# Kernel optimization log

Hardware: AMD Instinct MI355X
Metric: run time of the kernel (lower is better)

The kernel has to match this reference:

```python
import jax, jax.numpy as jnp
import numpy as np

DIM = 1024
N_EXPERTS = 8
TOPK = 2
INTER = 1408
SHARED_INTER = 2 * INTER  # n_shared_experts * moe_inter_dim
BATCH, SEQ = 2, 1024


def setup_inputs() -> dict:
    key = jax.random.key(0)
    ks = jax.random.split(key, 16)
    s = 0.02
    f32 = jnp.float32
    return {
        "x": jax.random.normal(ks[0], (BATCH, SEQ, DIM), f32),
        # gate
        "gate_w": jax.random.normal(ks[1], (N_EXPERTS, DIM), f32) * s,
        "gate_b": jnp.zeros((N_EXPERTS,), f32),
        # stacked routed-expert weights (nn.Linear layout: [out, in])
        "w1": jax.random.normal(ks[2], (N_EXPERTS, INTER, DIM), f32) * s,
        "b1": jnp.zeros((N_EXPERTS, INTER), f32),
        "w2": jax.random.normal(ks[3], (N_EXPERTS, DIM, INTER), f32) * s,
        "b2": jnp.zeros((N_EXPERTS, DIM), f32),
        "w3": jax.random.normal(ks[4], (N_EXPERTS, INTER, DIM), f32) * s,
        "b3": jnp.zeros((N_EXPERTS, INTER), f32),
        # shared-expert MLP
        "sw1": jax.random.normal(ks[5], (SHARED_INTER, DIM), f32) * s,
        "sb1": jnp.zeros((SHARED_INTER,), f32),
        "sw2": jax.random.normal(ks[6], (DIM, SHARED_INTER), f32) * s,
        "sb2": jnp.zeros((DIM,), f32),
        "sw3": jax.random.normal(ks[7], (SHARED_INTER, DIM), f32) * s,
        "sb3": jnp.zeros((SHARED_INTER,), f32),
    }


def reference(x, gate_w, gate_b, w1, b1, w2, b2, w3, b3,
              sw1, sb1, sw2, sb2, sw3, sb3):
    shape = x.shape
    xf = x.reshape(-1, shape[-1])  # [T, D]

    # Gate (returns full probs + top-k indices, matching source)
    scores = xf @ gate_w.T + gate_b                      # [T, E]
    probs = jax.nn.softmax(scores, axis=-1)              # [T, E]
    _, idx = jax.lax.top_k(probs, TOPK)                  # [T, K] int32

    # Faithful to `weights[mask].sum(dim=1)` where weights == full probs
    scale = probs.sum(axis=-1, keepdims=True)            # [T, 1] (== 1 for softmax)

    # dispatch[t, e] = token t routed to expert e
    dispatch = (idx[:, :, None] == jnp.arange(N_EXPERTS)[None, None, :]).any(axis=1)  # [T, E]

    # Dense per-expert SwiGLU (mask-combine mirrors the source's masked loop)
    h1 = jnp.einsum('td,eid->tei', xf, w1) + b1          # [T, E, I]
    h3 = jnp.einsum('td,eid->tei', xf, w3) + b3          # [T, E, I]
    out = jnp.einsum('tei,edi->ted', jax.nn.silu(h1) * h3, w2) + b2  # [T, E, D]
    y = jnp.where(dispatch[:, :, None], out, 0.0).sum(axis=1) * scale  # [T, D]

    # Shared-expert MLP
    z = (jax.nn.silu(xf @ sw1.T + sb1) * (xf @ sw3.T + sb3)) @ sw2.T + sb2  # [T, D]

    return probs, idx, (y + z).reshape(shape)
```

## Files before the change

### kernel.cpp

```cpp
#include <hip/hip_runtime.h>
#include <math.h>

static constexpr int TOK    = 2048;
static constexpr int DIM_   = 1024;
static constexpr int NE     = 8;
static constexpr int INTER_ = 1408;
static constexpr int SINT   = 2816;
static constexpr int NSLOT  = TOK * 2;

static constexpr size_t XB_OFF   = 0;
static constexpr size_t HR_OFF   = XB_OFF   + (size_t)TOK * DIM_ * 2;
static constexpr size_t HS_OFF   = HR_OFF   + (size_t)NSLOT * INTER_ * 2;
static constexpr size_t YS_OFF   = HS_OFF   + (size_t)TOK * SINT * 2;
static constexpr size_t ZP_OFF   = YS_OFF   + (size_t)NSLOT * DIM_ * 2;
static constexpr size_t W1B_OFF  = ZP_OFF   + (size_t)2 * TOK * DIM_ * 4;
static constexpr size_t W3B_OFF  = W1B_OFF  + (size_t)NE * INTER_ * DIM_ * 2;
static constexpr size_t W2B_OFF  = W3B_OFF  + (size_t)NE * INTER_ * DIM_ * 2;
static constexpr size_t SW1B_OFF = W2B_OFF  + (size_t)NE * DIM_ * INTER_ * 2;
static constexpr size_t SW3B_OFF = SW1B_OFF + (size_t)SINT * DIM_ * 2;
static constexpr size_t SW2B_OFF = SW3B_OFF + (size_t)SINT * DIM_ * 2;
static constexpr size_t TOPK_OFF = SW2B_OFF + (size_t)DIM_ * SINT * 2;
static constexpr size_t SCALE_OFF= TOPK_OFF + (size_t)TOK * 2 * 4;
static constexpr size_t SLOT_OFF = SCALE_OFF+ (size_t)TOK * 4;
static constexpr size_t ROWT_OFF = SLOT_OFF + (size_t)TOK * 2 * 4;
static constexpr size_t WL_OFF   = ROWT_OFF + (size_t)NSLOT * 4 + 1024;

typedef unsigned short u16;
typedef u16   u16x4  __attribute__((ext_vector_type(4)));
typedef u16   u16x8  __attribute__((ext_vector_type(8)));
typedef __bf16 bf16x8 __attribute__((ext_vector_type(8)));
typedef float f32x4  __attribute__((ext_vector_type(4)));

static __device__ __forceinline__ u16 f2bf(float f) {
  unsigned int u = __builtin_bit_cast(unsigned int, f);
  return (u16)((u + 0x7fffu + ((u >> 16) & 1u)) >> 16);
}
static __device__ __forceinline__ float bf2f(u16 h) {
  unsigned int u = ((unsigned int)h) << 16;
  return __builtin_bit_cast(float, u);
}
static __device__ __forceinline__ f32x4 mfma16(u16x8 a, u16x8 b, f32x4 c) {
  return __builtin_amdgcn_mfma_f32_16x16x32_bf16(
      __builtin_bit_cast(bf16x8, a), __builtin_bit_cast(bf16x8, b), c, 0, 0, 0);
}
static __device__ __forceinline__ void gload16(const void* g, void* l) {
  __builtin_amdgcn_global_load_lds(
      (const __attribute__((address_space(1))) unsigned int*)g,
      (__attribute__((address_space(3))) unsigned int*)l, 16, 0, 0);
}
#define WAITV(N) asm volatile("s_waitcnt vmcnt(" #N ")" ::: "memory")

__global__ __launch_bounds__(256) void gate_conv_kernel(
    const float* __restrict__ x, const float* __restrict__ gw,
    const float* __restrict__ gb,
    const float* __restrict__ w1, const float* __restrict__ w3,
    const float* __restrict__ sw1, const float* __restrict__ sw3,
    u16* __restrict__ xb, u16* __restrict__ w1b, u16* __restrict__ w3b,
    u16* __restrict__ sw1b, u16* __restrict__ sw3b,
    float* __restrict__ probs_out, float* __restrict__ idx_out,
    int* __restrict__ topk, float* __restrict__ scalep)
{
  const int tid = threadIdx.x;
  if (blockIdx.x >= 512) {
    int g = blockIdx.x - 512;
    const float* src; u16* dst;
    if      (g < 2816) {            src = w1;  dst = w1b;  }
    else if (g < 5632) { g -= 2816; src = w3;  dst = w3b;  }
    else if (g < 6336) { g -= 5632; src = sw1; dst = sw1b; }
    else               { g -= 6336; src = sw3; dst = sw3b; }
    const size_t base = (size_t)g * 4096 + (size_t)tid * 16;
    #pragma unroll
    for (int j = 0; j < 4; ++j) {
      float4 v = *(const float4*)(src + base + j * 4);
      *(u16x4*)(dst + base + j * 4) =
          (u16x4){ f2bf(v.x), f2bf(v.y), f2bf(v.z), f2bf(v.w) };
    }
    return;
  }
  {
    const size_t base = (size_t)blockIdx.x * 4096 + (size_t)tid * 16;
    const float4* src = (const float4*)(x + base);
    u16* dst = xb + base;
    #pragma unroll
    for (int j = 0; j < 4; ++j) {
      float4 v = src[j];
      *(u16x4*)(dst + j * 4) = (u16x4){ f2bf(v.x), f2bf(v.y), f2bf(v.z), f2bf(v.w) };
    }
  }
  const int wid = tid >> 6, lane = tid & 63;
  const int t = blockIdx.x * 4 + wid;
  const float* xr = x + (size_t)t * DIM_;
  double part[NE] = {0,0,0,0,0,0,0,0};
  for (int it = 0; it < DIM_ / 64; ++it) {
    const int d = lane + it * 64;
    const double xv = (double)xr[d];
    #pragma unroll
    for (int e = 0; e < NE; ++e) part[e] += xv * (double)gw[e * DIM_ + d];
  }
  #pragma unroll
  for (int e = 0; e < NE; ++e) {
    #pragma unroll
    for (int off = 32; off; off >>= 1) part[e] += __shfl_xor(part[e], off);
    part[e] += (double)gb[e];
  }
  if (lane == 0) {
    double m = part[0];
    #pragma unroll
    for (int e = 1; e < NE; ++e) m = fmax(m, part[e]);
    double p[NE], sd = 0.0;
    #pragma unroll
    for (int e = 0; e < NE; ++e) { p[e] = exp(part[e] - m); sd += p[e]; }
    float pf[NE]; float sumf = 0.0f;
    #pragma unroll
    for (int e = 0; e < NE; ++e) { pf[e] = (float)(p[e] / sd); sumf += pf[e]; }
    int a0 = 0;
    #pragma unroll
    for (int e = 1; e < NE; ++e) if (part[e] > part[a0]) a0 = e;
    int a1 = (a0 == 0) ? 1 : 0;
    #pragma unroll
    for (int e = 0; e < NE; ++e) if (e != a0 && part[e] > part[a1]) a1 = e;
    #pragma unroll
    for (int e = 0; e < NE; ++e) probs_out[t * NE + e] = pf[e];
    idx_out[t * 2 + 0] = (float)a0;
    idx_out[t * 2 + 1] = (float)a1;
    topk[t * 2 + 0] = a0; topk[t * 2 + 1] = a1;
    scalep[t] = sumf;
  }
}

__global__ __launch_bounds__(256) void plan_kernel(
    const int* __restrict__ topk, int4* __restrict__ wl,
    int* __restrict__ row_token, int* __restrict__ slot_of)
{
  __shared__ int pc[256][NE];
  __shared__ int base[NE], tot[NE];
  const int tid = threadIdx.x;
  int loc[NE] = {0,0,0,0,0,0,0,0};
  #pragma unroll 1
  for (int i = 0; i < 16; ++i) ++loc[topk[tid * 16 + i]];
  #pragma unroll
  for (int e = 0; e < NE; ++e) pc[tid][e] = loc[e];
  __syncthreads();
  if (tid < NE) {
    int acc = 0;
    for (int th = 0; th < 256; ++th) { int v = pc[th][tid]; pc[th][tid] = acc; acc += v; }
    tot[tid] = acc;
  }
  __syncthreads();
  if (tid == 0) {
    int acc = 0;
    for (int e = 0; e < NE; ++e) { base[e] = acc; acc += tot[e]; }
    int n = 0;
    for (int e = 0; e < NE; ++e)
      for (int r = 0; r < tot[e]; r += 256)
        wl[n++] = make_int4(e, base[e] + r, min(256, tot[e] - r), 0);
    for (int h = 0; h < 2; ++h)
      for (int mt = 0; mt < 8; ++mt)
        wl[n++] = make_int4(NE + h, mt * 256, 256, 0);
    for (int i = n; i < 64; ++i) wl[i] = make_int4(-1, 0, 0, 0);
  }
  __syncthreads();
  int pos[NE];
  #pragma unroll
  for (int e = 0; e < NE; ++e) pos[e] = base[e] + pc[tid][e];
  #pragma unroll 1
  for (int i = 0; i < 16; ++i) {
    const int gi = tid * 16 + i;
    const int e = topk[gi];
    const int s = pos[e]++;
    row_token[s] = gi >> 1;
    slot_of[gi] = s;
  }
}

__global__ __launch_bounds__(512) void g13_kernel(
    const u16* __restrict__ xb, const int* __restrict__ row_token,
    const int4* __restrict__ wl,
    const u16* __restrict__ w1b, const float* __restrict__ b1,
    const u16* __restrict__ w3b, const float* __restrict__ b3,
    const u16* __restrict__ sw1b, const float* __restrict__ sb1,
    const u16* __restrict__ sw3b, const float* __restrict__ sb3,
    u16* __restrict__ Hr, u16* __restrict__ Hs,
    const float* __restrict__ w2f, const float* __restrict__ sw2f,
    u16* __restrict__ w2b, u16* __restrict__ sw2b)
{
  constexpr int K = DIM_;
  constexpr int NT = K / 32;
  const int tid = threadIdx.x, wid = tid >> 6, lane = tid & 63;

  if (blockIdx.y >= 40) {
    const int cid = (blockIdx.y - 40) * 22 + blockIdx.x;
    for (int chunk = cid; chunk < 1760; chunk += 176) {
      int g = chunk; const float* src; u16* dst;
      if (g < 1408) { src = w2f;  dst = w2b;  }
      else { g -= 1408; src = sw2f; dst = sw2b; }
      const size_t base = (size_t)g * 8192 + (size_t)tid * 16;
      #pragma unroll
      for (int j = 0; j < 4; ++j) {
        float4 v = *(const float4*)(src + base + j * 4);
        *(u16x4*)(dst + base + j * 4) =
            (u16x4){ f2bf(v.x), f2bf(v.y), f2bf(v.z), f2bf(v.w) };
      }
    }
    return;
  }

  const int4 it = wl[blockIdx.y];
  const int z = it.x;
  if (z < 0) return;
  const int rowbase = it.y, rows_lim = it.z;
  const int col0 = blockIdx.x * 64;

  const int lrow = lane >> 2;
  const int sce = ((lane & 3) ^ ((lane >> 3) & 3)) * 8;

  const u16 *W1, *W3; const float *B1p, *B3p;
  u16* Hbase; int ldh;
  const u16* aptr[2];

  if (z < NE) {
    #pragma unroll
    for (int q = 0; q < 2; ++q) {
      const int rq = wid * 32 + q * 16 + lrow;
      const int t = (rq < rows_lim) ? row_token[rowbase + rq] : 0;
      aptr[q] = xb + (size_t)t * K + sce;
    }
    W1 = w1b + (size_t)z * INTER_ * K;  W3 = w3b + (size_t)z * INTER_ * K;
    B1p = b1 + z * INTER_;              B3p = b3 + z * INTER_;
    Hbase = Hr + (size_t)rowbase * INTER_;  ldh = INTER_;
  } else {
    const int h = z - NE;
    #pragma unroll
    for (int q = 0; q < 2; ++q) {
      const int rq = wid * 32 + q * 16 + lrow;
      aptr[q] = xb + (size_t)(rowbase + min(rq, rows_lim - 1)) * K + sce;
    }
    W1 = sw1b + (size_t)h * INTER_ * K;  W3 = sw3b + (size_t)h * INTER_ * K;
    B1p = sb1 + h * INTER_;              B3p = sb3 + h * INTER_;
    Hbase = Hs + (size_t)rowbase * SINT + h * INTER_;  ldh = SINT;
  }

  __shared__ alignas(16) u16 Al [2][256 * 32];
  __shared__ alignas(16) u16 B1l[2][64 * 32];
  __shared__ alignas(16) u16 B3l[2][64 * 32];

  const int brole = wid >> 2, bw = wid & 3;
  const u16* bsrc = (brole ? W3 : W1) + (size_t)(col0 + bw * 16 + lrow) * K + sce;
  u16* bdst0 = brole ? &B3l[0][bw * 512] : &B1l[0][bw * 512];
  u16* bdst1 = brole ? &B3l[1][bw * 512] : &B1l[1][bw * 512];

  #define G13_STAGE(p, kt) {                                          \
    const int k0_ = (kt) * 32;                                        \
    gload16(aptr[0] + k0_, &Al[p][(wid * 2 + 0) * 512]);              \
    gload16(aptr[1] + k0_, &Al[p][(wid * 2 + 1) * 512]);              \
    gload16(bsrc + k0_, (p) ? bdst1 : bdst0);                         \
  }

  G13_STAGE(0, 0);

  const int wr = wid >> 1, wc = wid & 1, fr = lane & 15, gr = lane >> 4;
  const int key = (fr >> 1) & 3;
  f32x4 acc1[4][2] = {}, acc3[4][2] = {};
  int p = 0;

  #pragma unroll 1
  for (int kt = 0; kt < NT; ++kt) {
    if (kt + 1 < NT) { G13_STAGE(p ^ 1, kt + 1); WAITV(3); }
    else             { WAITV(0); }
    __builtin_amdgcn_s_barrier();
    u16x8 af[4], b1f[2], b3f[2];
    #pragma unroll
    for (int mi = 0; mi < 4; ++mi)
      af[mi] = *(const u16x8*)&Al[p][(wr * 64 + mi * 16 + fr) * 32 + ((gr ^ key) * 8)];
    #pragma unroll
    for (int ni = 0; ni < 2; ++ni) {
      const int off = (wc * 32 + ni * 16 + fr) * 32 + ((gr ^ key) * 8);
      b1f[ni] = *(const u16x8*)&B1l[p][off];
      b3f[ni] = *(const u16x8*)&B3l[p][off];
    }
    __builtin_amdgcn_s_setprio(1);
    #pragma unroll
    for (int mi = 0; mi < 4; ++mi)
      #pragma unroll
      for (int ni = 0; ni < 2; ++ni) {
        acc1[mi][ni] = mfma16(af[mi], b1f[ni], acc1[mi][ni]);
        acc3[mi][ni] = mfma16(af[mi], b3f[ni], acc3[mi][ni]);
      }
    __builtin_amdgcn_s_setprio(0);
    __builtin_amdgcn_s_barrier();
    p ^= 1;
  }
  #undef G13_STAGE

  #pragma unroll
  for (int ni = 0; ni < 2; ++ni) {
    const int gcol = col0 + wc * 32 + ni * 16 + fr;
    const float bb1 = B1p[gcol], bb3 = B3p[gcol];
    #pragma unroll
    for (int mi = 0; mi < 4; ++mi) {
      const int rb = wr * 64 + mi * 16 + gr * 4;
      #pragma unroll
      for (int j = 0; j < 4; ++j) {
        const int r = rb + j;
        if (r < rows_lim) {
          const float h1 = acc1[mi][ni][j] + bb1;
          const float h3 = acc3[mi][ni][j] + bb3;
          const float hv = (h1 / (1.0f + __expf(-h1))) * h3;
          Hbase[(size_t)r * ldh + gcol] = f2bf(hv);
        }
      }
    }
  }
}

__global__ __launch_bounds__(512) void g2_kernel(
    const u16* __restrict__ Hr, const u16* __restrict__ Hs,
    const int4* __restrict__ wl,
    const u16* __restrict__ w2b, const float* __restrict__ b2,
    const u16* __restrict__ sw2b,
    u16* __restrict__ Ys, float* __restrict__ Zp)
{
  constexpr int NT = INTER_ / 32;
  const int4 it = wl[blockIdx.y];
  const int z = it.x;
  if (z < 0) return;
  const int rowbase = it.y, rows_lim = it.z;
  const int col0 = blockIdx.x * 128;

  const int tid = threadIdx.x, wid = tid >> 6, lane = tid & 63;
  const int lrow = lane >> 2;
  const int sce = ((lane & 3) ^ ((lane >> 3) & 3)) * 8;

  const u16 *Abase, *W; const float* BB;
  int ldA, ldW;
  u16* Yout = nullptr; float* Zout = nullptr;
  if (z < NE) {
    Abase = Hr + (size_t)rowbase * INTER_;  ldA = INTER_;
    W = w2b + (size_t)z * DIM_ * INTER_;    ldW = INTER_;
    BB = b2 + z * DIM_;
    Yout = Ys + (size_t)rowbase * DIM_;
  } else {
    const int h = z - NE;
    Abase = Hs + (size_t)rowbase * SINT + h * INTER_;  ldA = SINT;
    W = sw2b + h * INTER_;                             ldW = SINT;
    BB = nullptr;
    Zout = Zp + (size_t)h * TOK * DIM_ + (size_t)rowbase * DIM_;
  }

  const u16* aptr[2];
  #pragma unroll
  for (int q = 0; q < 2; ++q) {
    const int rq = wid * 32 + q * 16 + lrow;
    aptr[q] = Abase + (size_t)min(rq, rows_lim - 1) * ldA + sce;
  }
  const u16* wsrc = W + (size_t)(col0 + wid * 16 + lrow) * ldW + sce;

  __shared__ alignas(16) u16 Al[3][256 * 32];
  __shared__ alignas(16) u16 Bl[3][128 * 32];

  #define G2_STAGE(p, kt) {                                           \
    const int k0_ = (kt) * 32;                                        \
    gload16(aptr[0] + k0_, &Al[p][(wid * 2 + 0) * 512]);              \
    gload16(aptr[1] + k0_, &Al[p][(wid * 2 + 1) * 512]);              \
    gload16(wsrc + k0_, &Bl[p][wid * 512]);                           \
  }

  G2_STAGE(0, 0);
  G2_STAGE(1, 1);

  const int wr = wid >> 1, wc = wid & 1, fr = lane & 15, gr = lane >> 4;
  const int key = (fr >> 1) & 3;
  f32x4 acc[4][4] = {};
  int cur = 0;

  #pragma unroll 1
  for (int kt = 0; kt < NT; ++kt) {
    if (kt + 1 < NT) { WAITV(3); }
    else             { WAITV(0); }
    __builtin_amdgcn_s_barrier();
    if (kt + 2 < NT) {
      const int nx = (cur + 2 >= 3) ? cur - 1 : cur + 2;
      G2_STAGE(nx, kt + 2);
    }
    u16x8 af[4], bf_[4];
    #pragma unroll
    for (int mi = 0; mi < 4; ++mi)
      af[mi] = *(const u16x8*)&Al[cur][(wr * 64 + mi * 16 + fr) * 32 + ((gr ^ key) * 8)];
    #pragma unroll
    for (int ni = 0; ni < 4; ++ni)
      bf_[ni] = *(const u16x8*)&Bl[cur][(wc * 64 + ni * 16 + fr) * 32 + ((gr ^ key) * 8)];
    __builtin_amdgcn_s_setprio(1);
    #pragma unroll
    for (int mi = 0; mi < 4; ++mi)
      #pragma unroll
      for (int ni = 0; ni < 4; ++ni)
        acc[mi][ni] = mfma16(af[mi], bf_[ni], acc[mi][ni]);
    __builtin_amdgcn_s_setprio(0);
    cur = (cur + 1 == 3) ? 0 : cur + 1;
  }
  #undef G2_STAGE

  #pragma unroll
  for (int ni = 0; ni < 4; ++ni) {
    const int gcol = col0 + wc * 64 + ni * 16 + fr;
    const float bb = BB ? BB[gcol] : 0.0f;
    #pragma unroll
    for (int mi = 0; mi < 4; ++mi) {
      const int rb = wr * 64 + mi * 16 + gr * 4;
      #pragma unroll
      for (int j = 0; j < 4; ++j) {
        const int r = rb + j;
        if (r < rows_lim) {
          const float val = acc[mi][ni][j] + bb;
          if (z < NE) Yout[(size_t)r * DIM_ + gcol] = f2bf(val);
          else        Zout[(size_t)r * DIM_ + gcol] = val;
        }
      }
    }
  }
}

__global__ __launch_bounds__(256) void combine_kernel(
    const u16* __restrict__ Ys, const float* __restrict__ Zp,
    const int* __restrict__ slot_of, const float* __restrict__ scalep,
    const float* __restrict__ sb2, float* __restrict__ y_out)
{
  const int t = blockIdx.x, c = threadIdx.x * 4;
  const int s0 = slot_of[t * 2], s1 = slot_of[t * 2 + 1];
  const float s = scalep[t];
  u16x4 a = *(const u16x4*)(Ys + (size_t)s0 * DIM_ + c);
  u16x4 b = *(const u16x4*)(Ys + (size_t)s1 * DIM_ + c);
  float4 z0 = *(const float4*)(Zp + (size_t)t * DIM_ + c);
  float4 z1 = *(const float4*)(Zp + (size_t)TOK * DIM_ + (size_t)t * DIM_ + c);
  float4 sb = *(const float4*)(sb2 + c);
  float4 o;
  o.x = (bf2f(a[0]) + bf2f(b[0])) * s + z0.x + z1.x + sb.x;
  o.y = (bf2f(a[1]) + bf2f(b[1])) * s + z0.y + z1.y + sb.y;
  o.z = (bf2f(a[2]) + bf2f(b[2])) * s + z0.z + z1.z + sb.z;
  o.w = (bf2f(a[3]) + bf2f(b[3])) * s + z0.w + z1.w + sb.w;
  *(float4*)(y_out + (size_t)t * DIM_ + c) = o;
}

extern "C" void kernel_launch(void* const* d_in, const int* in_sizes, int n_in,
                              void* d_out, int out_size, void* d_ws, size_t ws_size,
                              hipStream_t stream) {
  (void)in_sizes; (void)n_in; (void)out_size; (void)ws_size;
  const float* x   = (const float*)d_in[0];
  const float* gw  = (const float*)d_in[1];
  const float* gb  = (const float*)d_in[2];
  const float* w1  = (const float*)d_in[3];
  const float* b1  = (const float*)d_in[4];
  const float* w2  = (const float*)d_in[5];
  const float* b2  = (const float*)d_in[6];
  const float* w3  = (const float*)d_in[7];
  const float* b3  = (const float*)d_in[8];
  const float* sw1 = (const float*)d_in[9];
  const float* sb1 = (const float*)d_in[10];
  const float* sw2 = (const float*)d_in[11];
  const float* sb2 = (const float*)d_in[12];
  const float* sw3 = (const float*)d_in[13];
  const float* sb3 = (const float*)d_in[14];

  float* out       = (float*)d_out;
  float* probs_out = out;
  float* idx_out   = out + TOK * NE;
  float* y_out     = out + TOK * NE + TOK * 2;

  char* ws = (char*)d_ws;
  u16*   xb        = (u16*)  (ws + XB_OFF);
  u16*   Hr        = (u16*)  (ws + HR_OFF);
  u16*   Hs        = (u16*)  (ws + HS_OFF);
  u16*   Ysl       = (u16*)  (ws + YS_OFF);
  float* Zp        = (float*)(ws + ZP_OFF);
  u16*   w1b       = (u16*)  (ws + W1B_OFF);
  u16*   w3b       = (u16*)  (ws + W3B_OFF);
  u16*   w2b       = (u16*)  (ws + W2B_OFF);
  u16*   sw1b      = (u16*)  (ws + SW1B_OFF);
  u16*   sw3b      = (u16*)  (ws + SW3B_OFF);
  u16*   sw2b      = (u16*)  (ws + SW2B_OFF);
  int*   topk      = (int*)  (ws + TOPK_OFF);
  float* scalep    = (float*)(ws + SCALE_OFF);
  int*   slot_of   = (int*)  (ws + SLOT_OFF);
  int*   row_token = (int*)  (ws + ROWT_OFF);
  int4*  wl        = (int4*) (ws + WL_OFF);

  gate_conv_kernel<<<512 + 7040, 256, 0, stream>>>(
      x, gw, gb, w1, w3, sw1, sw3,
      xb, w1b, w3b, sw1b, sw3b,
      probs_out, idx_out, topk, scalep);
  plan_kernel<<<1, 256, 0, stream>>>(topk, wl, row_token, slot_of);
  g13_kernel<<<dim3(22, 48), 512, 0, stream>>>(
      xb, row_token, wl, w1b, b1, w3b, b3, sw1b, sb1, sw3b, sb3, Hr, Hs,
      w2, sw2, w2b, sw2b);
  g2_kernel<<<dim3(8, 40), 512, 0, stream>>>(
      Hr, Hs, wl, w2b, b2, sw2b, Ysl, Zp);
  combine_kernel<<<TOK, 256, 0, stream>>>(Ysl, Zp, slot_of, scalep, sb2, y_out);
}
```

Before: 196.5 us.

## Fuse combine into down-projection via atomic adds with split-K work list

```diff
diff --git a/kernel.cpp b/kernel.cpp
--- a/kernel.cpp
+++ b/kernel.cpp
@@ -7,13 +7,12 @@
 static constexpr int INTER_ = 1408;
 static constexpr int SINT   = 2816;
 static constexpr int NSLOT  = TOK * 2;
+static constexpr int KC     = 704;
 
 static constexpr size_t XB_OFF   = 0;
 static constexpr size_t HR_OFF   = XB_OFF   + (size_t)TOK * DIM_ * 2;
 static constexpr size_t HS_OFF   = HR_OFF   + (size_t)NSLOT * INTER_ * 2;
-static constexpr size_t YS_OFF   = HS_OFF   + (size_t)TOK * SINT * 2;
-static constexpr size_t ZP_OFF   = YS_OFF   + (size_t)NSLOT * DIM_ * 2;
-static constexpr size_t W1B_OFF  = ZP_OFF   + (size_t)2 * TOK * DIM_ * 4;
+static constexpr size_t W1B_OFF  = HS_OFF   + (size_t)TOK * SINT * 2;
 static constexpr size_t W3B_OFF  = W1B_OFF  + (size_t)NE * INTER_ * DIM_ * 2;
 static constexpr size_t W2B_OFF  = W3B_OFF  + (size_t)NE * INTER_ * DIM_ * 2;
 static constexpr size_t SW1B_OFF = W2B_OFF  + (size_t)NE * DIM_ * INTER_ * 2;
@@ -24,6 +23,7 @@
 static constexpr size_t SLOT_OFF = SCALE_OFF+ (size_t)TOK * 4;
 static constexpr size_t ROWT_OFF = SLOT_OFF + (size_t)TOK * 2 * 4;
 static constexpr size_t WL_OFF   = ROWT_OFF + (size_t)NSLOT * 4 + 1024;
+static constexpr size_t WL2_OFF  = WL_OFF   + 48 * 16;
 
 typedef unsigned short u16;
 typedef u16   u16x4  __attribute__((ext_vector_type(4)));
@@ -58,7 +58,8 @@
     u16* __restrict__ xb, u16* __restrict__ w1b, u16* __restrict__ w3b,
     u16* __restrict__ sw1b, u16* __restrict__ sw3b,
     float* __restrict__ probs_out, float* __restrict__ idx_out,
-    int* __restrict__ topk, float* __restrict__ scalep)
+    int* __restrict__ topk, float* __restrict__ scalep,
+    float* __restrict__ y_out)
 {
   const int tid = threadIdx.x;
   if (blockIdx.x >= 512) {
@@ -78,6 +79,12 @@
     return;
   }
   {
+    float4 z4 = {0.f, 0.f, 0.f, 0.f};
+    float* yz = y_out + (size_t)blockIdx.x * 4096 + (size_t)tid * 16;
+    #pragma unroll
+    for (int j = 0; j < 4; ++j) *(float4*)(yz + j * 4) = z4;
+  }
+  {
     const size_t base = (size_t)blockIdx.x * 4096 + (size_t)tid * 16;
     const float4* src = (const float4*)(x + base);
     u16* dst = xb + base;
@@ -129,7 +136,8 @@
 }
 
 __global__ __launch_bounds__(256) void plan_kernel(
-    const int* __restrict__ topk, int4* __restrict__ wl,
+    const int* __restrict__ topk, int4* __restrict__ wl13,
+    int4* __restrict__ wl2,
     int* __restrict__ row_token, int* __restrict__ slot_of)
 {
   __shared__ int pc[256][NE];
@@ -153,11 +161,20 @@
     int n = 0;
     for (int e = 0; e < NE; ++e)
       for (int r = 0; r < tot[e]; r += 256)
-        wl[n++] = make_int4(e, base[e] + r, min(256, tot[e] - r), 0);
+        wl13[n++] = make_int4(e, base[e] + r, min(256, tot[e] - r), 0);
     for (int h = 0; h < 2; ++h)
       for (int mt = 0; mt < 8; ++mt)
-        wl[n++] = make_int4(NE + h, mt * 256, 256, 0);
-    for (int i = n; i < 64; ++i) wl[i] = make_int4(-1, 0, 0, 0);
+        wl13[n++] = make_int4(NE + h, mt * 256, 256, 0);
+    for (int i = n; i < 48; ++i) wl13[i] = make_int4(-1, 0, 0, 0);
+    int n2 = 0;
+    for (int e = 0; e < NE; ++e)
+      for (int r = 0; r < tot[e]; r += 256)
+        for (int kh = 0; kh < 2; ++kh)
+          wl2[n2++] = make_int4(e, base[e] + r, min(256, tot[e] - r), kh);
+    for (int q = 0; q < 4; ++q)
+      for (int mt = 0; mt < 8; ++mt)
+        wl2[n2++] = make_int4(NE, mt * 256, 256, q);
+    for (int i = n2; i < 80; ++i) wl2[i] = make_int4(-1, 0, 0, 0);
   }
   __syncthreads();
   int pos[NE];
@@ -315,36 +332,32 @@
 
 __global__ __launch_bounds__(512) void g2_kernel(
     const u16* __restrict__ Hr, const u16* __restrict__ Hs,
-    const int4* __restrict__ wl,
+    const int4* __restrict__ wl2, const int* __restrict__ row_token,
+    const float* __restrict__ scalep,
     const u16* __restrict__ w2b, const float* __restrict__ b2,
-    const u16* __restrict__ sw2b,
-    u16* __restrict__ Ys, float* __restrict__ Zp)
+    const u16* __restrict__ sw2b, const float* __restrict__ sb2,
+    float* __restrict__ y_out)
 {
-  constexpr int NT = INTER_ / 32;
-  const int4 it = wl[blockIdx.y];
+  constexpr int NT = KC / 32;
+  const int4 it = wl2[blockIdx.y];
   const int z = it.x;
   if (z < 0) return;
-  const int rowbase = it.y, rows_lim = it.z;
+  const int rowbase = it.y, rows_lim = it.z, kq = it.w;
   const int col0 = blockIdx.x * 128;
 
   const int tid = threadIdx.x, wid = tid >> 6, lane = tid & 63;
   const int lrow = lane >> 2;
   const int sce = ((lane & 3) ^ ((lane >> 3) & 3)) * 8;
 
-  const u16 *Abase, *W; const float* BB;
+  const u16 *Abase, *W;
   int ldA, ldW;
-  u16* Yout = nullptr; float* Zout = nullptr;
-  if (z < NE) {
-    Abase = Hr + (size_t)rowbase * INTER_;  ldA = INTER_;
-    W = w2b + (size_t)z * DIM_ * INTER_;    ldW = INTER_;
-    BB = b2 + z * DIM_;
-    Yout = Ys + (size_t)rowbase * DIM_;
+  const bool routed = (z < NE);
+  if (routed) {
+    Abase = Hr + (size_t)rowbase * INTER_ + kq * KC;          ldA = INTER_;
+    W = w2b + (size_t)z * DIM_ * INTER_ + kq * KC;            ldW = INTER_;
   } else {
-    const int h = z - NE;
-    Abase = Hs + (size_t)rowbase * SINT + h * INTER_;  ldA = SINT;
-    W = sw2b + h * INTER_;                             ldW = SINT;
-    BB = nullptr;
-    Zout = Zp + (size_t)h * TOK * DIM_ + (size_t)rowbase * DIM_;
+    Abase = Hs + (size_t)rowbase * SINT + kq * KC;            ldA = SINT;
+    W = sw2b + kq * KC;                                       ldW = SINT;
   }
 
   const u16* aptr[2];
@@ -403,7 +416,8 @@
   #pragma unroll
   for (int ni = 0; ni < 4; ++ni) {
     const int gcol = col0 + wc * 64 + ni * 16 + fr;
-    const float bb = BB ? BB[gcol] : 0.0f;
+    float bb = 0.0f;
+    if (kq == 0) bb = routed ? b2[z * DIM_ + gcol] : sb2[gcol];
     #pragma unroll
     for (int mi = 0; mi < 4; ++mi) {
       const int rb = wr * 64 + mi * 16 + gr * 4;
@@ -411,34 +425,18 @@
       for (int j = 0; j < 4; ++j) {
         const int r = rb + j;
         if (r < rows_lim) {
-          const float val = acc[mi][ni][j] + bb;
-          if (z < NE) Yout[(size_t)r * DIM_ + gcol] = f2bf(val);
-          else        Zout[(size_t)r * DIM_ + gcol] = val;
+          if (routed) {
+            const int tok = row_token[rowbase + r];
+            atomicAdd(&y_out[(size_t)tok * DIM_ + gcol],
+                      (acc[mi][ni][j] + bb) * scalep[tok]);
+          } else {
+            atomicAdd(&y_out[(size_t)(rowbase + r) * DIM_ + gcol],
+                      acc[mi][ni][j] + bb);
+          }
         }
       }
     }
   }
-}
-
-__global__ __launch_bounds__(256) void combine_kernel(
-    const u16* __restrict__ Ys, const float* __restrict__ Zp,
-    const int* __restrict__ slot_of, const float* __restrict__ scalep,
-    const float* __restrict__ sb2, float* __restrict__ y_out)
-{
-  const int t = blockIdx.x, c = threadIdx.x * 4;
-  const int s0 = slot_of[t * 2], s1 = slot_of[t * 2 + 1];
-  const float s = scalep[t];
-  u16x4 a = *(const u16x4*)(Ys + (size_t)s0 * DIM_ + c);
-  u16x4 b = *(const u16x4*)(Ys + (size_t)s1 * DIM_ + c);
-  float4 z0 = *(const float4*)(Zp + (size_t)t * DIM_ + c);
-  float4 z1 = *(const float4*)(Zp + (size_t)TOK * DIM_ + (size_t)t * DIM_ + c);
-  float4 sb = *(const float4*)(sb2 + c);
-  float4 o;
-  o.x = (bf2f(a[0]) + bf2f(b[0])) * s + z0.x + z1.x + sb.x;
-  o.y = (bf2f(a[1]) + bf2f(b[1])) * s + z0.y + z1.y + sb.y;
-  o.z = (bf2f(a[2]) + bf2f(b[2])) * s + z0.z + z1.z + sb.z;
-  o.w = (bf2f(a[3]) + bf2f(b[3])) * s + z0.w + z1.w + sb.w;
-  *(float4*)(y_out + (size_t)t * DIM_ + c) = o;
 }
 
 extern "C" void kernel_launch(void* const* d_in, const int* in_sizes, int n_in,
@@ -470,8 +468,6 @@
   u16*   xb        = (u16*)  (ws + XB_OFF);
   u16*   Hr        = (u16*)  (ws + HR_OFF);
   u16*   Hs        = (u16*)  (ws + HS_OFF);
-  u16*   Ysl       = (u16*)  (ws + YS_OFF);
-  float* Zp        = (float*)(ws + ZP_OFF);
   u16*   w1b       = (u16*)  (ws + W1B_OFF);
   u16*   w3b       = (u16*)  (ws + W3B_OFF);
   u16*   w2b       = (u16*)  (ws + W2B_OFF);
@@ -482,17 +478,17 @@
   float* scalep    = (float*)(ws + SCALE_OFF);
   int*   slot_of   = (int*)  (ws + SLOT_OFF);
   int*   row_token = (int*)  (ws + ROWT_OFF);
-  int4*  wl        = (int4*) (ws + WL_OFF);
+  int4*  wl13      = (int4*) (ws + WL_OFF);
+  int4*  wl2       = (int4*) (ws + WL2_OFF);
 
   gate_conv_kernel<<<512 + 7040, 256, 0, stream>>>(
       x, gw, gb, w1, w3, sw1, sw3,
       xb, w1b, w3b, sw1b, sw3b,
-      probs_out, idx_out, topk, scalep);
-  plan_kernel<<<1, 256, 0, stream>>>(topk, wl, row_token, slot_of);
+      probs_out, idx_out, topk, scalep, y_out);
+  plan_kernel<<<1, 256, 0, stream>>>(topk, wl13, wl2, row_token, slot_of);
   g13_kernel<<<dim3(22, 48), 512, 0, stream>>>(
-      xb, row_token, wl, w1b, b1, w3b, b3, sw1b, sb1, sw3b, sb3, Hr, Hs,
+      xb, row_token, wl13, w1b, b1, w3b, b3, sw1b, sb1, sw3b, sb3, Hr, Hs,
       w2, sw2, w2b, sw2b);
-  g2_kernel<<<dim3(8, 40), 512, 0, stream>>>(
-      Hr, Hs, wl, w2b, b2, sw2b, Ysl, Zp);
-  combine_kernel<<<TOK, 256, 0, stream>>>(Ysl, Zp, slot_of, scalep, sb2, y_out);
-}
+  g2_kernel<<<dim3(8, 80), 512, 0, stream>>>(
+      Hr, Hs, wl2, row_token, scalep, w2b, b2, sw2b, sb2, y_out);
+}
```

Result: slower. 241.6 us (+22.9%).

## Fuse W1/W3 bf16 conversion into g13 GEMM by loading fp32 weights directly

Applied to the files above, without the earlier changes.

```diff
diff --git a/kernel.cpp b/kernel.cpp
--- a/kernel.cpp
+++ b/kernel.cpp
@@ -13,12 +13,8 @@
 static constexpr size_t HS_OFF   = HR_OFF   + (size_t)NSLOT * INTER_ * 2;
 static constexpr size_t YS_OFF   = HS_OFF   + (size_t)TOK * SINT * 2;
 static constexpr size_t ZP_OFF   = YS_OFF   + (size_t)NSLOT * DIM_ * 2;
-static constexpr size_t W1B_OFF  = ZP_OFF   + (size_t)2 * TOK * DIM_ * 4;
-static constexpr size_t W3B_OFF  = W1B_OFF  + (size_t)NE * INTER_ * DIM_ * 2;
-static constexpr size_t W2B_OFF  = W3B_OFF  + (size_t)NE * INTER_ * DIM_ * 2;
-static constexpr size_t SW1B_OFF = W2B_OFF  + (size_t)NE * DIM_ * INTER_ * 2;
-static constexpr size_t SW3B_OFF = SW1B_OFF + (size_t)SINT * DIM_ * 2;
-static constexpr size_t SW2B_OFF = SW3B_OFF + (size_t)SINT * DIM_ * 2;
+static constexpr size_t W2B_OFF  = ZP_OFF   + (size_t)2 * TOK * DIM_ * 4;
+static constexpr size_t SW2B_OFF = W2B_OFF  + (size_t)NE * DIM_ * INTER_ * 2;
 static constexpr size_t TOPK_OFF = SW2B_OFF + (size_t)DIM_ * SINT * 2;
 static constexpr size_t SCALE_OFF= TOPK_OFF + (size_t)TOK * 2 * 4;
 static constexpr size_t SLOT_OFF = SCALE_OFF+ (size_t)TOK * 4;
@@ -39,6 +35,11 @@
   unsigned int u = ((unsigned int)h) << 16;
   return __builtin_bit_cast(float, u);
 }
+static __device__ __forceinline__ unsigned int cvtpk(float lo, float hi) {
+  unsigned int r;
+  asm("v_cvt_pk_bf16_f32 %0, %1, %2" : "=v"(r) : "v"(lo), "v"(hi));
+  return r;
+}
 static __device__ __forceinline__ f32x4 mfma16(u16x8 a, u16x8 b, f32x4 c) {
   return __builtin_amdgcn_mfma_f32_16x16x32_bf16(
       __builtin_bit_cast(bf16x8, a), __builtin_bit_cast(bf16x8, b), c, 0, 0, 0);
@@ -50,33 +51,13 @@
 }
 #define WAITV(N) asm volatile("s_waitcnt vmcnt(" #N ")" ::: "memory")
 
-__global__ __launch_bounds__(256) void gate_conv_kernel(
+__global__ __launch_bounds__(256) void gate_kernel(
     const float* __restrict__ x, const float* __restrict__ gw,
-    const float* __restrict__ gb,
-    const float* __restrict__ w1, const float* __restrict__ w3,
-    const float* __restrict__ sw1, const float* __restrict__ sw3,
-    u16* __restrict__ xb, u16* __restrict__ w1b, u16* __restrict__ w3b,
-    u16* __restrict__ sw1b, u16* __restrict__ sw3b,
+    const float* __restrict__ gb, u16* __restrict__ xb,
     float* __restrict__ probs_out, float* __restrict__ idx_out,
     int* __restrict__ topk, float* __restrict__ scalep)
 {
   const int tid = threadIdx.x;
-  if (blockIdx.x >= 512) {
-    int g = blockIdx.x - 512;
-    const float* src; u16* dst;
-    if      (g < 2816) {            src = w1;  dst = w1b;  }
-    else if (g < 5632) { g -= 2816; src = w3;  dst = w3b;  }
-    else if (g < 6336) { g -= 5632; src = sw1; dst = sw1b; }
-    else               { g -= 6336; src = sw3; dst = sw3b; }
-    const size_t base = (size_t)g * 4096 + (size_t)tid * 16;
-    #pragma unroll
-    for (int j = 0; j < 4; ++j) {
-      float4 v = *(const float4*)(src + base + j * 4);
-      *(u16x4*)(dst + base + j * 4) =
-          (u16x4){ f2bf(v.x), f2bf(v.y), f2bf(v.z), f2bf(v.w) };
-    }
-    return;
-  }
   {
     const size_t base = (size_t)blockIdx.x * 4096 + (size_t)tid * 16;
     const float4* src = (const float4*)(x + base);
@@ -176,10 +157,10 @@
 __global__ __launch_bounds__(512) void g13_kernel(
     const u16* __restrict__ xb, const int* __restrict__ row_token,
     const int4* __restrict__ wl,
-    const u16* __restrict__ w1b, const float* __restrict__ b1,
-    const u16* __restrict__ w3b, const float* __restrict__ b3,
-    const u16* __restrict__ sw1b, const float* __restrict__ sb1,
-    const u16* __restrict__ sw3b, const float* __restrict__ sb3,
+    const float* __restrict__ w1, const float* __restrict__ b1,
+    const float* __restrict__ w3, const float* __restrict__ b3,
+    const float* __restrict__ sw1, const float* __restrict__ sb1,
+    const float* __restrict__ sw3, const float* __restrict__ sb3,
     u16* __restrict__ Hr, u16* __restrict__ Hs,
     const float* __restrict__ w2f, const float* __restrict__ sw2f,
     u16* __restrict__ w2b, u16* __restrict__ sw2b)
@@ -214,7 +195,7 @@
   const int lrow = lane >> 2;
   const int sce = ((lane & 3) ^ ((lane >> 3) & 3)) * 8;
 
-  const u16 *W1, *W3; const float *B1p, *B3p;
+  const float *W1, *W3, *B1p, *B3p;
   u16* Hbase; int ldh;
   const u16* aptr[2];
 
@@ -225,8 +206,8 @@
       const int t = (rq < rows_lim) ? row_token[rowbase + rq] : 0;
       aptr[q] = xb + (size_t)t * K + sce;
     }
-    W1 = w1b + (size_t)z * INTER_ * K;  W3 = w3b + (size_t)z * INTER_ * K;
-    B1p = b1 + z * INTER_;              B3p = b3 + z * INTER_;
+    W1 = w1 + (size_t)z * INTER_ * K;  W3 = w3 + (size_t)z * INTER_ * K;
+    B1p = b1 + z * INTER_;             B3p = b3 + z * INTER_;
     Hbase = Hr + (size_t)rowbase * INTER_;  ldh = INTER_;
   } else {
     const int h = z - NE;
@@ -235,37 +216,45 @@
       const int rq = wid * 32 + q * 16 + lrow;
       aptr[q] = xb + (size_t)(rowbase + min(rq, rows_lim - 1)) * K + sce;
     }
-    W1 = sw1b + (size_t)h * INTER_ * K;  W3 = sw3b + (size_t)h * INTER_ * K;
-    B1p = sb1 + h * INTER_;              B3p = sb3 + h * INTER_;
+    W1 = sw1 + (size_t)h * INTER_ * K;  W3 = sw3 + (size_t)h * INTER_ * K;
+    B1p = sb1 + h * INTER_;             B3p = sb3 + h * INTER_;
     Hbase = Hs + (size_t)rowbase * SINT + h * INTER_;  ldh = SINT;
   }
 
-  __shared__ alignas(16) u16 Al [2][256 * 32];
-  __shared__ alignas(16) u16 B1l[2][64 * 32];
-  __shared__ alignas(16) u16 B3l[2][64 * 32];
+  __shared__ alignas(16) u16   Al [2][256 * 32];
+  __shared__ alignas(16) float B1f[2][64 * 32];
+  __shared__ alignas(16) float B3f[2][64 * 32];
 
   const int brole = wid >> 2, bw = wid & 3;
-  const u16* bsrc = (brole ? W3 : W1) + (size_t)(col0 + bw * 16 + lrow) * K + sce;
-  u16* bdst0 = brole ? &B3l[0][bw * 512] : &B1l[0][bw * 512];
-  u16* bdst1 = brole ? &B3l[1][bw * 512] : &B1l[1][bw * 512];
-
-  #define G13_STAGE(p, kt) {                                          \
-    const int k0_ = (kt) * 32;                                        \
-    gload16(aptr[0] + k0_, &Al[p][(wid * 2 + 0) * 512]);              \
-    gload16(aptr[1] + k0_, &Al[p][(wid * 2 + 1) * 512]);              \
-    gload16(bsrc + k0_, (p) ? bdst1 : bdst0);                         \
+  const float* Wb = brole ? W3 : W1;
+  const float* bsrcf[2];
+  #pragma unroll
+  for (int l = 0; l < 2; ++l) {
+    const int idx = lane + l * 64;
+    bsrcf[l] = Wb + (size_t)(col0 + bw * 16 + (idx >> 3)) * K
+                  + (((idx & 7) ^ ((idx >> 3) & 7)) * 4);
+  }
+
+  #define G13_STAGE(p, kt) {                                            \
+    const int k0_ = (kt) * 32;                                          \
+    gload16(aptr[0] + k0_, &Al[p][(wid * 2 + 0) * 512]);                \
+    gload16(aptr[1] + k0_, &Al[p][(wid * 2 + 1) * 512]);                \
+    float* bb_ = brole ? &B3f[p][bw * 512] : &B1f[p][bw * 512];         \
+    gload16(bsrcf[0] + k0_, bb_ + lane * 4);                            \
+    gload16(bsrcf[1] + k0_, bb_ + (lane + 64) * 4);                     \
   }
 
   G13_STAGE(0, 0);
 
   const int wr = wid >> 1, wc = wid & 1, fr = lane & 15, gr = lane >> 4;
   const int key = (fr >> 1) & 3;
+  const int keyb = fr & 7;
   f32x4 acc1[4][2] = {}, acc3[4][2] = {};
   int p = 0;
 
   #pragma unroll 1
   for (int kt = 0; kt < NT; ++kt) {
-    if (kt + 1 < NT) { G13_STAGE(p ^ 1, kt + 1); WAITV(3); }
+    if (kt + 1 < NT) { G13_STAGE(p ^ 1, kt + 1); WAITV(4); }
     else             { WAITV(0); }
     __builtin_amdgcn_s_barrier();
     u16x8 af[4], b1f[2], b3f[2];
@@ -274,9 +263,22 @@
       af[mi] = *(const u16x8*)&Al[p][(wr * 64 + mi * 16 + fr) * 32 + ((gr ^ key) * 8)];
     #pragma unroll
     for (int ni = 0; ni < 2; ++ni) {
-      const int off = (wc * 32 + ni * 16 + fr) * 32 + ((gr ^ key) * 8);
-      b1f[ni] = *(const u16x8*)&B1l[p][off];
-      b3f[ni] = *(const u16x8*)&B3l[p][off];
+      const int rb = wc * 32 + ni * 16 + fr;
+      const int c0 = (2 * gr) ^ keyb;
+      const int c1 = c0 ^ 1;
+      const float* p1 = &B1f[p][rb * 32];
+      const float* p3 = &B3f[p][rb * 32];
+      f32x4 lo1 = *(const f32x4*)(p1 + c0 * 4);
+      f32x4 hi1 = *(const f32x4*)(p1 + c1 * 4);
+      f32x4 lo3 = *(const f32x4*)(p3 + c0 * 4);
+      f32x4 hi3 = *(const f32x4*)(p3 + c1 * 4);
+      uint4 t1, t3;
+      t1.x = cvtpk(lo1[0], lo1[1]); t1.y = cvtpk(lo1[2], lo1[3]);
+      t1.z = cvtpk(hi1[0], hi1[1]); t1.w = cvtpk(hi1[2], hi1[3]);
+      t3.x = cvtpk(lo3[0], lo3[1]); t3.y = cvtpk(lo3[2], lo3[3]);
+      t3.z = cvtpk(hi3[0], hi3[1]); t3.w = cvtpk(hi3[2], hi3[3]);
+      b1f[ni] = __builtin_bit_cast(u16x8, t1);
+      b3f[ni] = __builtin_bit_cast(u16x8, t3);
     }
     __builtin_amdgcn_s_setprio(1);
     #pragma unroll
@@ -472,11 +474,7 @@
   u16*   Hs        = (u16*)  (ws + HS_OFF);
   u16*   Ysl       = (u16*)  (ws + YS_OFF);
   float* Zp        = (float*)(ws + ZP_OFF);
-  u16*   w1b       = (u16*)  (ws + W1B_OFF);
-  u16*   w3b       = (u16*)  (ws + W3B_OFF);
   u16*   w2b       = (u16*)  (ws + W2B_OFF);
-  u16*   sw1b      = (u16*)  (ws + SW1B_OFF);
-  u16*   sw3b      = (u16*)  (ws + SW3B_OFF);
   u16*   sw2b      = (u16*)  (ws + SW2B_OFF);
   int*   topk      = (int*)  (ws + TOPK_OFF);
   float* scalep    = (float*)(ws + SCALE_OFF);
@@ -484,13 +482,11 @@
   int*   row_token = (int*)  (ws + ROWT_OFF);
   int4*  wl        = (int4*) (ws + WL_OFF);
 
-  gate_conv_kernel<<<512 + 7040, 256, 0, stream>>>(
-      x, gw, gb, w1, w3, sw1, sw3,
-      xb, w1b, w3b, sw1b, sw3b,
-      probs_out, idx_out, topk, scalep);
+  gate_kernel<<<512, 256, 0, stream>>>(x, gw, gb, xb, probs_out, idx_out,
+                                       topk, scalep);
   plan_kernel<<<1, 256, 0, stream>>>(topk, wl, row_token, slot_of);
   g13_kernel<<<dim3(22, 48), 512, 0, stream>>>(
-      xb, row_token, wl, w1b, b1, w3b, b3, sw1b, sb1, sw3b, sb3, Hr, Hs,
+      xb, row_token, wl, w1, b1, w3, b3, sw1, sb1, sw3, sb3, Hr, Hs,
       w2, sw2, w2b, sw2b);
   g2_kernel<<<dim3(8, 40), 512, 0, stream>>>(
       Hr, Hs, wl, w2b, b2, sw2b, Ysl, Zp);
```

After: 194.5 us. No clear change (-1.0%).
